# Kernel optimization log

Measured on AMD Instinct MI355X. Metric: run time of the kernel, lower is better.

Reference implementation:

```python
import jax, jax.numpy as jnp
import numpy as np

NCODONS = 100
ORDER = 2
ALPH = 4
N_STATES = 6 * NCODONS + 12            # calc_number_of_states()
N_TRANS = 3 * NCODONS + 5              # calc_number_of_transition_parameters()
N_EMIT_COLS = 6 ** (ORDER + 1)         # 216, per build()
N_OBS_SYMBOLS = (ALPH + 1) ** (ORDER + 1) + 1  # 126 order-transformed symbols


def _transition_structure(n):
    """Static sparse structure of the transition matrix (indices) and the
    delete-transition hop distances, exactly mirroring
    get_indices_and_values_from_transition_kernel_higher_order."""
    idx = [[0, 0], [0, 1], [1, 2], [2, 3]]
    idx += [[3 + i * 3, 4 + i * 3] for i in range(n)]
    idx += [[4 + i * 3, 5 + i * 3] for i in range(n)]
    idx += [[5 + i * 3, 6 + i * 3] for i in range(n)]
    off = 8 + 3 * n                      # first insert state
    idx += [[3 + i * 3, off + i * 3] for i in range(n + 1)]
    idx += [[3 + n * 3, 4 + n * 3]]
    idx += [[off + i * 3, off + 1 + i * 3] for i in range(n + 1)]
    idx += [[off + 1 + i * 3, off + 2 + i * 3] for i in range(n + 1)]
    idx += [[off + 2 + i * 3, 4 + i * 3] for i in range(n + 1)]
    idx += [[off + 2 + i * 3, off + i * 3] for i in range(n + 1)]
    i_del = [3 + i * 3 for i in range(n) for j in range(n - i)]
    j_del = [4 + j * 3 for i in range(1, n + 1) for j in range(i, n + 1)]
    idx += [[a, b] for a, b in zip(i_del, j_del)]
    idx += [[4 + n * 3, 5 + n * 3], [5 + n * 3, 6 + n * 3], [6 + n * 3, 7 + n * 3]]
    t1 = 8 + n * 3 + (n + 1) * 3         # terminal-1 state
    idx += [[7 + n * 3, 7 + n * 3], [7 + n * 3, t1], [t1, t1]]
    d = np.array([(b - a) // 3 for a, b in zip(i_del, j_del)], np.int32)
    return np.array(idx, np.int32), d

TRANS_IDX, DEL_HOPS = _transition_structure(NCODONS)


def _transition_values(w, n):
    """Values paired 1:1 with TRANS_IDX, same order as the original code."""
    wk = w[3 * n + 4]                    # shared delete parameter
    ones = lambda m: jnp.ones((m,), w.dtype)
    return jnp.concatenate([
        jnp.stack([1 - w[0], w[0]]),     # [0,0],[0,1]
        ones(2),                         # [1,2],[2,3]
        w[1:1 + n],                      # codon entries
        ones(2 * n),                     # codon chain x2
        w[1 + n:2 + 2 * n],              # inserts (n+1)
        w[2 + 2 * n:3 + 2 * n],          # last-codon -> stop
        ones(2 * (n + 1)),               # insert chains x2
        w[3 + 2 * n:4 + 3 * n],          # insert exit (n+1)
        1 - w[3 + 2 * n:4 + 3 * n],      # insert self-loop (n+1)
        1 - wk ** (jnp.asarray(DEL_HOPS) + 1),  # delete transitions
        ones(6),                         # stop chain + terminal loops
    ])


def make_A(transition_kernel):
    """Dense transition matrix after tf.sparse.softmax semantics:
    softmax over the structurally-nonzero entries of each row only."""
    vals = _transition_values(transition_kernel, NCODONS)
    logits = jnp.full((N_STATES, N_STATES), -jnp.inf, transition_kernel.dtype)
    logits = logits.at[TRANS_IDX[:, 0], TRANS_IDX[:, 1]].set(vals)
    return jax.nn.softmax(logits, axis=1)  # exp(-inf)=0 off-structure


def _forward_loglik(ids, transition_kernel, emission_kernel, init_kernel):
    A = make_A(transition_kernel)                                   # [S,S]
    E = jax.nn.softmax(emission_kernel.reshape(N_STATES, -1), axis=1)  # [S,216]
    Et = E.T                                                        # [216,S]
    pi = jax.nn.softmax(init_kernel)                                # [S]
    obs = ids.T                                                     # [T,B]

    a0 = pi[None, :] * Et[obs[0]]                                   # [B,S]
    s0 = a0.sum(-1, keepdims=True)
    carry0 = (a0 / s0, jnp.log(s0[..., 0]))

    def step(carry, ob):
        alpha, ll = carry
        a = (alpha @ A) * Et[ob]                                    # [B,S]
        s = a.sum(-1, keepdims=True)
        return (a / s, ll + jnp.log(s[..., 0])), None

    (alpha, ll), _ = jax.lax.scan(step, carry0, obs[1:])
    return ll                                                       # [B]


def setup_inputs() -> dict:
    key = jax.random.key(0)
    k1, k2, k3, k4 = jax.random.split(key, 4)
    ids = jax.random.randint(k1, (32, 2048), 0, N_OBS_SYMBOLS, dtype=jnp.int32)
    transition_kernel = 0.05 * jax.random.normal(k2, (N_TRANS,), jnp.float32)
    emission_kernel = 0.05 * jax.random.normal(k3, (N_STATES * N_EMIT_COLS,), jnp.float32)
    init_kernel = 0.05 * jax.random.normal(k4, (N_STATES,), jnp.float32)
    return {"ids": ids, "transition_kernel": transition_kernel,
            "emission_kernel": emission_kernel, "init_kernel": init_kernel}


def reference(ids, transition_kernel, emission_kernel, init_kernel):
    return _forward_loglik(ids, transition_kernel, emission_kernel, init_kernel)
```

## Files before the change

kernel.cpp:

```cpp
#include <hip/hip_runtime.h>
#include <math.h>

#define NS 612
#define NECOL 216
#define BATCH 32
#define TLEN 2048
#define ROWW 1024
#define CE 2.7182818284590452f

#define O_AV0 0
#define O_AV1 128
#define O_BV0 256
#define O_BV1 384
#define O_IZ3 512
#define O_SC  640
#define O_PIP 768
#define O_ET  2048

typedef float f32x4 __attribute__((ext_vector_type(4)));
typedef int   i32x2 __attribute__((ext_vector_type(2)));

__device__ __forceinline__ int eslot(int s) {
  if (s >= 4 && s <= 306)  { int i = (s - 4) / 3,  r = (s - 4) % 3;
    return (i >> 1) * 16 + (i & 1) * 6 + r; }
  if (s >= 308 && s <= 610){ int i = (s - 308) / 3, r = (s - 308) % 3;
    return (i >> 1) * 16 + (i & 1) * 6 + 3 + r; }
  if (s <= 3)   return (60 + s) * 16 + 12;
  if (s == 307) return 51 * 16 + 12;
  return 52 * 16 + 12;
}

#define DPPF(x, ctrl, rm) __int_as_float(__builtin_amdgcn_update_dpp(0, __float_as_int(x), (ctrl), (rm), 0xf, true))

__device__ __forceinline__ float scan_plain(float x) {
  x += DPPF(x, 0x111, 0xf);
  x += DPPF(x, 0x112, 0xf);
  x += DPPF(x, 0x114, 0xf);
  x += DPPF(x, 0x118, 0xf);
  x += DPPF(x, 0x142, 0xa);
  x += DPPF(x, 0x143, 0xc);
  return x;
}
__device__ __forceinline__ float wshr1(float x) { return DPPF(x, 0x138, 0xf); }
__device__ __forceinline__ float ror1(float x)  { return DPPF(x, 0x13C, 0xf); }
__device__ __forceinline__ float rdl(float x, int l) {
  return __int_as_float(__builtin_amdgcn_readlane(__float_as_int(x), l));
}

__global__ void k_prep(const float* __restrict__ w, float* __restrict__ ws) {
  __shared__ float Gs[101];
  int tid = threadIdx.x;
  float wk = w[304];
  if (tid >= 1 && tid <= 100) {
    float p = wk;
    for (int k = 0; k < tid; ++k) p *= wk;
    Gs[tid] = expf(1.f - p);
  }
  if (tid == 0) {
    Gs[0] = 0.f;
    ws[O_SC + 0] = wk;
    float Z0 = expf(1.f - w[0]) + expf(w[0]);
    ws[O_SC + 1] = expf(1.f - w[0]) / Z0;
    ws[O_SC + 2] = expf(w[0]) / Z0;
  }
  __syncthreads();
  if (tid <= 100) {
    float em = expf(w[tid < 100 ? 1 + tid : 202]);
    float ei = expf(w[101 + tid]);
    float z = em + ei;
    for (int d = 1; d <= 100 - tid; ++d) z += Gs[d];
    float ex = expf(w[203 + tid]);
    float es = expf(1.f - w[203 + tid]);
    float z310 = ex + es;
    ws[O_AV0 + tid] = em / z;
    ws[O_BV0 + tid] = ei / z;
    ws[O_AV1 + tid] = ex / z310;
    ws[O_BV1 + tid] = es / z310;
    ws[O_IZ3 + tid] = 1.f / z;
  }
}

__global__ void k_zr(float* __restrict__ ws) {
  float* row = ws + O_ET + (size_t)blockIdx.x * ROWW;
  for (int i = threadIdx.x; i < ROWW; i += 256) row[i] = 0.f;
}

__global__ void k_et(const float* __restrict__ ek, float* __restrict__ ws) {
  float* Etp = ws + O_ET;
  int s = blockIdx.x;
  int lane = threadIdx.x;
  int sl = eslot(s);
  float x[4]; float m = -1e30f;
  #pragma unroll
  for (int k = 0; k < 4; ++k) {
    int c = lane + 64 * k;
    x[k] = (c < NECOL) ? ek[s * NECOL + c] : -1e30f;
    m = fmaxf(m, x[k]);
  }
  #pragma unroll
  for (int o = 32; o; o >>= 1) m = fmaxf(m, __shfl_xor(m, o, 64));
  float e[4]; float sum = 0.f;
  #pragma unroll
  for (int k = 0; k < 4; ++k) {
    int c = lane + 64 * k;
    e[k] = (c < NECOL) ? expf(x[k] - m) : 0.f;
    sum += e[k];
  }
  #pragma unroll
  for (int o = 32; o; o >>= 1) sum += __shfl_xor(sum, o, 64);
  float inv = 1.f / sum;
  #pragma unroll
  for (int k = 0; k < 4; ++k) {
    int c = lane + 64 * k;
    if (c < NECOL) Etp[(size_t)c * ROWW + sl] = e[k] * inv;
  }
}

__global__ void k_pi(const float* __restrict__ ik, float* __restrict__ ws) {
  float* pip = ws + O_PIP;
  __shared__ float wm[10], wsm[10];
  int tid = threadIdx.x;
  for (int i = tid; i < ROWW; i += 640) pip[i] = 0.f;
  __syncthreads();
  int lane = tid & 63, wid = tid >> 6;
  float x = (tid < NS) ? ik[tid] : -1e30f;
  float m = x;
  #pragma unroll
  for (int o = 32; o; o >>= 1) m = fmaxf(m, __shfl_xor(m, o, 64));
  if (lane == 0) wm[wid] = m;
  __syncthreads();
  float mm = wm[0];
  #pragma unroll
  for (int k = 1; k < 10; ++k) mm = fmaxf(mm, wm[k]);
  float e = (tid < NS) ? expf(x - mm) : 0.f;
  float sacc = e;
  #pragma unroll
  for (int o = 32; o; o >>= 1) sacc += __shfl_xor(sacc, o, 64);
  if (lane == 0) wsm[wid] = sacc;
  __syncthreads();
  float ss = 0.f;
  #pragma unroll
  for (int k = 0; k < 10; ++k) ss += wsm[k];
  if (tid < NS) pip[eslot(tid)] = e / ss;
}

__global__ __launch_bounds__(64, 1) void k_main(const int* __restrict__ ids,
                                                const float* __restrict__ ws,
                                                float* __restrict__ out) {
  const int L = threadIdx.x, b = blockIdx.x;
  const int* idsb = ids + b * TLEN;
  const float* Etp = ws + O_ET;
  const float* pip = ws + O_PIP;
  const unsigned long long Et64 = (unsigned long long)Etp;
  const unsigned long long ids64 = (unsigned long long)idsb;
  const int voff = L << 6;

  int ie = 2 * L;     if (ie > 100) ie = 100;
  int io = 2 * L + 1; if (io > 100) io = 100;
  float AV0e = ws[O_AV0 + ie], AV1e = ws[O_AV1 + ie];
  float BV0e = ws[O_BV0 + ie], BV1e = ws[O_BV1 + ie];
  float AV0o = ws[O_AV0 + io], AV1o = ws[O_AV1 + io];
  float BV0o = ws[O_BV0 + io], BV1o = ws[O_BV1 + io];
  float izeCE = ((2 * L <= 99)     ? ws[O_IZ3 + 2 * L]     : 0.f) * CE;
  float izoCE = ((2 * L + 1 <= 99) ? ws[O_IZ3 + 2 * L + 1] : 0.f) * CE;
  float wk  = ws[O_SC + 0], A00 = ws[O_SC + 1], A01 = ws[O_SC + 2];

  float k0 = 0.f, k1 = 0.f, kx = 0.f;
  if (L == 61) k0 = A01;
  else if (L == 62 || L == 63) k0 = 1.f;
  else if (L == 52) k0 = 0.5f;
  if (L == 60) k1 = A00;
  else if (L == 51) { k1 = 0.5f; kx = 1.f; }
  else if (L == 52) k1 = 1.f;
  const bool isL0 = (L == 0);

  const float sk1 = 1.f - wk;
  const float r2 = wk * wk;
  const float q1 = r2, q2 = r2 * r2;

  int ob0 = __builtin_amdgcn_readfirstlane(idsb[0]);
  const float* R0 = Etp + (size_t)ob0 * ROWW;
  f32x4 p0 = *(const f32x4*)(pip + L * 16);
  f32x4 p1 = *(const f32x4*)(pip + L * 16 + 4);
  f32x4 p2 = *(const f32x4*)(pip + L * 16 + 8);
  float p3 = pip[L * 16 + 12];
  f32x4 e0 = *(const f32x4*)(R0 + L * 16);
  f32x4 e1 = *(const f32x4*)(R0 + L * 16 + 4);
  f32x4 e2 = *(const f32x4*)(R0 + L * 16 + 8);
  float e3 = R0[L * 16 + 12];

  float c4e = p0.x * e0.x, c5e = p0.y * e0.y, c6e = p0.z * e0.z, i8e = p0.w * e0.w;
  float i9e = p1.x * e1.x, i10e = p1.y * e1.y, c4o = p1.z * e1.z, c5o = p1.w * e1.w;
  float c6o = p2.x * e2.x, i8o = p2.y * e2.y, i9o = p2.z * e2.z, i10o = p2.w * e2.w;
  float spv = p3 * e3;

  float Sp, Tp, mdo;
  {
    float sprd0 = ror1(spv);
    float pme = isL0 ? sprd0 : ror1(c6o);
    float mde = pme * izeCE;
    mdo = c6e * izoCE;
    Sp = scan_plain(mde + mdo);
    float v1 = fmaf(wk, mde, mdo);
    float t1 = wshr1(v1), t2 = wshr1(t1);
    Tp = fmaf(q2, t2, fmaf(q1, t1, v1));
  }

  int e_acc = 0;

#define STEP_BODY(B0, B1, B2, B3) do { \
    float De = fmaf(-r2, wshr1(Tp), wshr1(Sp)); \
    float Do = fmaf(-wk, Tp, Sp); Do = fmaf(-sk1, mdo, Do); \
    float exc  = ror1(c6e); \
    float sprd = ror1(spv); \
    float pve = isL0 ? sprd : ror1(c6o); \
    float pvo = c6e; \
    float t4e = fmaf(AV0e, pve, fmaf(AV1e, i10e, De)) * (B0).x; \
    float t5e = c4e * (B0).y; \
    float t6e = c5e * (B0).z; \
    float t8e = fmaf(BV0e, pve, BV1e * i10e) * (B0).w; \
    float t9e = i8e * (B1).x; \
    float tXe = i9e * (B1).y; \
    float t4o = fmaf(AV0o, pvo, fmaf(AV1o, i10o, Do)) * (B1).z; \
    float t5o = c4o * (B1).w; \
    float t6o = c5o * (B2).x; \
    float t8o = fmaf(BV0o, pvo, BV1o * i10o) * (B2).y; \
    float t9o = i8o * (B2).z; \
    float tXo = i9o * (B2).w; \
    float nsp = fmaf(kx, exc, fmaf(k0, sprd, k1 * spv)) * (B3); \
    c4e = t4e; c5e = t5e; c6e = t6e; i8e = t8e; i9e = t9e; i10e = tXe; \
    c4o = t4o; c5o = t5o; c6o = t6o; i8o = t8o; i9o = t9o; i10o = tXo; \
    spv = nsp; \
    float sprdn = ror1(spv); \
    float pmn = isL0 ? sprdn : ror1(c6o); \
    float mde = pmn * izeCE; \
    mdo = c6e * izoCE; \
    Sp = scan_plain(mde + mdo); \
    float v1 = fmaf(wk, mde, mdo); \
    float t1 = wshr1(v1), t2 = wshr1(t1); \
    Tp = fmaf(q2, t2, fmaf(q1, t1, v1)); \
  } while (0)

#define FUSE2(R1a, R1b, R1c, R1d, R2a, R2b, R2c, R2d) do { \
     \
    float De = fmaf(-r2, wshr1(Tp), wshr1(Sp)); \
    float Do = fmaf(-wk, Tp, Sp); Do = fmaf(-sk1, mdo, Do); \
    float exc  = ror1(c6e); \
    float sprd = ror1(spv); \
    float pve = isL0 ? sprd : ror1(c6o); \
    float pvo = c6e; \
    float a4e = fmaf(AV0e, pve, fmaf(AV1e, i10e, De)) * (R1a).x; \
    float a5e = c4e * (R1a).y; \
    float a6e = c5e * (R1a).z; \
    float a8e = fmaf(BV0e, pve, BV1e * i10e) * (R1a).w; \
    float a9e = i8e * (R1b).x; \
    float aXe = i9e * (R1b).y; \
    float a4o = fmaf(AV0o, pvo, fmaf(AV1o, i10o, Do)) * (R1b).z; \
    float a5o = c4o * (R1b).w; \
    float a6o = c5o * (R1c).x; \
    float a8o = fmaf(BV0o, pvo, BV1o * i10o) * (R1c).y; \
    float a9o = i8o * (R1c).z; \
    float aXo = i9o * (R1c).w; \
    float asp = fmaf(kx, exc, fmaf(k0, sprd, k1 * spv)) * (R1d); \
     \
    float b5e = a4e * (R2a).y; \
    float b6e = a5e * (R2a).z; \
    float b9e = a8e * (R2b).x; \
    float bXe = a9e * (R2b).y; \
    float b5o = a4o * (R2b).w; \
    float b6o = a5o * (R2c).x; \
    float b9o = a8o * (R2c).z; \
    float bXo = a9o * (R2c).w; \
    float excb  = ror1(a6e); \
    float bsprd = ror1(asp); \
    float bsp = fmaf(kx, excb, fmaf(k0, bsprd, k1 * asp)) * (R2d); \
    float pma = isL0 ? bsprd : ror1(a6o); \
    float mdea = pma * izeCE; \
    float mdoa = a6e * izoCE; \
    float csprd = ror1(bsp); \
    float pmb = isL0 ? csprd : ror1(b6o); \
    float mdeb = pmb * izeCE; \
    float mdob = b6e * izoCE; \
    float Sa = mdea + mdoa, Ta0 = fmaf(wk, mdea, mdoa); \
    float Sb = mdeb + mdob, Tb0 = fmaf(wk, mdeb, mdob); \
     \
    Sa += DPPF(Sa, 0x111, 0xf); Sb += DPPF(Sb, 0x111, 0xf); \
    float ta1 = wshr1(Ta0); float tb1 = wshr1(Tb0); \
    Sa += DPPF(Sa, 0x112, 0xf); Sb += DPPF(Sb, 0x112, 0xf); \
    float ta2 = wshr1(ta1); float tb2 = wshr1(tb1); \
    Sa += DPPF(Sa, 0x114, 0xf); Sb += DPPF(Sb, 0x114, 0xf); \
    float Ta = fmaf(q2, ta2, fmaf(q1, ta1, Ta0)); \
    float Tb = fmaf(q2, tb2, fmaf(q1, tb1, Tb0)); \
    Sa += DPPF(Sa, 0x118, 0xf); Sb += DPPF(Sb, 0x118, 0xf); \
    Sa += DPPF(Sa, 0x142, 0xa); Sb += DPPF(Sb, 0x142, 0xa); \
    Sa += DPPF(Sa, 0x143, 0xc); Sb += DPPF(Sb, 0x143, 0xc); \
     \
    float Deb = fmaf(-r2, wshr1(Ta), wshr1(Sa)); \
    float Dob = fmaf(-wk, Ta, Sa); Dob = fmaf(-sk1, mdoa, Dob); \
    float b4e = fmaf(AV0e, pma, fmaf(AV1e, aXe, Deb)) * (R2a).x; \
    float b8e = fmaf(BV0e, pma, BV1e * aXe) * (R2a).w; \
    float b4o = fmaf(AV0o, a6e, fmaf(AV1o, aXo, Dob)) * (R2b).z; \
    float b8o = fmaf(BV0o, a6e, BV1o * aXo) * (R2c).y; \
     \
    c4e = b4e; c5e = b5e; c6e = b6e; i8e = b8e; i9e = b9e; i10e = bXe; \
    c4o = b4o; c5o = b5o; c6o = b6o; i8o = b8o; i9o = b9o; i10o = bXo; \
    spv = bsp; \
    Sp = Sb; Tp = Tb; mdo = mdob; \
  } while (0)

#define RESCALE() do { \
    float prr = ((c4e + c5e) + (c6e + i8e)) + ((i9e + i10e) + (c4o + c5o)) \
              + ((c6o + i8o) + (i9o + i10o)) + spv; \
    float ssum = rdl(scan_plain(prr), 63); \
    int exq = ((__float_as_int(ssum) >> 23) & 255) - 127; \
    e_acc += exq; \
    float scq = __int_as_float((127 - exq) << 23); \
    c4e *= scq; c5e *= scq; c6e *= scq; i8e *= scq; i9e *= scq; i10e *= scq; \
    c4o *= scq; c5o *= scq; c6o *= scq; i8o *= scq; i9o *= scq; i10o *= scq; \
    spv *= scq; \
    mdo *= scq; Sp *= scq; Tp *= scq; \
  } while (0)

#define GLD4(dst, base, off) \
  asm volatile("global_load_dwordx4 %0, %1, %2 offset:" #off \
               : "=v"(dst) : "v"(voff), "s"(base))
#define GLD1(dst, base, off) \
  asm volatile("global_load_dword %0, %1, %2 offset:" #off \
               : "=v"(dst) : "v"(voff), "s"(base))
#define GLD2(dst, base, vo, off) \
  asm volatile("global_load_dwordx2 %0, %1, %2 offset:" #off \
               : "=v"(dst) : "v"(vo), "s"(base))

#define LOADROW(P, obsv) do { \
    unsigned int _oc = (unsigned int)__builtin_amdgcn_readfirstlane(obsv); \
    unsigned long long _ba = Et64 + ((unsigned long long)_oc << 12); \
    GLD4(P##0, _ba, 0); \
    GLD4(P##1, _ba, 16); \
    GLD4(P##2, _ba, 32); \
    GLD1(P##3, _ba, 48); \
  } while (0)

#define LOADOBS(O, tstart) do { \
    int _ts = (tstart); if (_ts > TLEN - 6) _ts = TLEN - 6; \
    int _vo = _ts * 4; \
    GLD2(O##0, ids64, _vo, 0); \
    GLD2(O##1, ids64, _vo, 8); \
    GLD2(O##2, ids64, _vo, 16); \
  } while (0)

  for (int t = 1; t <= 7; ++t) {
    int obp = idsb[t];
    const float* Rx = Etp + (size_t)__builtin_amdgcn_readfirstlane(obp) * ROWW;
    f32x4 P0 = *(const f32x4*)(Rx + L * 16);
    f32x4 P1 = *(const f32x4*)(Rx + L * 16 + 4);
    f32x4 P2 = *(const f32x4*)(Rx + L * 16 + 8);
    float P3 = Rx[L * 16 + 12];
    STEP_BODY(P0, P1, P2, P3);
  }
  RESCALE();

  f32x4 Ar00, Ar01, Ar02; float Ar03;
  f32x4 Ar10, Ar11, Ar12; float Ar13;
  f32x4 Ar20, Ar21, Ar22; float Ar23;
  f32x4 Ar30, Ar31, Ar32; float Ar33;
  f32x4 Ar40, Ar41, Ar42; float Ar43;
  f32x4 Ar50, Ar51, Ar52; float Ar53;
  f32x4 Br00, Br01, Br02; float Br03;
  f32x4 Br10, Br11, Br12; float Br13;
  f32x4 Br20, Br21, Br22; float Br23;
  f32x4 Br30, Br31, Br32; float Br33;
  f32x4 Br40, Br41, Br42; float Br43;
  f32x4 Br50, Br51, Br52; float Br53;
  i32x2 OA0, OA1, OA2, OB0, OB1, OB2;

  LOADOBS(OA, 8);
  asm volatile("s_waitcnt vmcnt(0)" ::: "memory");
  __builtin_amdgcn_sched_barrier(0);
  LOADROW(Ar0, OA0.x);
  LOADROW(Ar1, OA0.y);
  LOADROW(Ar2, OA1.x);
  LOADROW(Ar3, OA1.y);
  LOADROW(Ar4, OA2.x);
  LOADROW(Ar5, OA2.y);
  LOADOBS(OB, 14);

#define ITER(C, OC, N, ON, gexp) do { \
    asm volatile("s_waitcnt vmcnt(0)" ::: "memory"); \
    __builtin_amdgcn_sched_barrier(0); \
    LOADROW(N##r0, (OC##0).x); \
    LOADROW(N##r1, (OC##0).y); \
    LOADROW(N##r2, (OC##1).x); \
    LOADROW(N##r3, (OC##1).y); \
    LOADROW(N##r4, (OC##2).x); \
    LOADROW(N##r5, (OC##2).y); \
    LOADOBS(ON, 8 + 6 * ((gexp) + 2)); \
    __builtin_amdgcn_sched_barrier(0); \
    FUSE2(C##r00, C##r01, C##r02, C##r03, C##r10, C##r11, C##r12, C##r13); \
    FUSE2(C##r20, C##r21, C##r22, C##r23, C##r30, C##r31, C##r32, C##r33); \
    FUSE2(C##r40, C##r41, C##r42, C##r43, C##r50, C##r51, C##r52, C##r53); \
  } while (0)

  for (int g = 0; g < 340; g += 2) {
    ITER(A, OB, B, OA, g);
    ITER(B, OA, A, OB, g + 1);
    RESCALE();
  }

  float prr = ((c4e + c5e) + (c6e + i8e)) + ((i9e + i10e) + (c4o + c5o))
            + ((c6o + i8o) + (i9o + i10o)) + spv;
  float ssum_f = rdl(scan_plain(prr), 63);
  double ll = (double)e_acc * 0.6931471805599453 + (double)logf(ssum_f);
  if (L == 0) out[b] = (float)ll;

#undef STEP_BODY
#undef FUSE2
#undef RESCALE
#undef GLD4
#undef GLD1
#undef GLD2
#undef LOADROW
#undef LOADOBS
#undef ITER
}

extern "C" void kernel_launch(void* const* d_in, const int* in_sizes, int n_in,
                              void* d_out, int out_size, void* d_ws, size_t ws_size,
                              hipStream_t stream) {
  const int*   ids = (const int*)d_in[0];
  const float* w   = (const float*)d_in[1];
  const float* ek  = (const float*)d_in[2];
  const float* ik  = (const float*)d_in[3];
  float* ws  = (float*)d_ws;
  float* out = (float*)d_out;

  k_prep<<<1, 128, 0, stream>>>(w, ws);
  k_zr  <<<NECOL, 256, 0, stream>>>(ws);
  k_pi  <<<1, 640, 0, stream>>>(ik, ws);
  k_et  <<<NS, 64, 0, stream>>>(ek, ws);
  k_main<<<BATCH, 64, 0, stream>>>(ids, ws, out);
}
```

Before: 299.0 us.

## Fuse three HMM time steps per block to batch the cross-lane scans

Replaces the two-step fused forward update with a three-step fusion. The three delete-path prefix scans (DPP adds and lane shifts) now run interleaved in one batch instead of two, which gives the serial dependency chain more instruction-level parallelism. The cost is higher register pressure from more live temporaries, and the step ordering is more intricate to get right.

```diff
diff --git a/kernel.cpp b/kernel.cpp
--- a/kernel.cpp
+++ b/kernel.cpp
@@ -241,27 +241,26 @@
     Tp = fmaf(q2, t2, fmaf(q1, t1, v1)); \
   } while (0)
 
-#define FUSE2(R1a, R1b, R1c, R1d, R2a, R2b, R2c, R2d) do { \
-     \
-    float De = fmaf(-r2, wshr1(Tp), wshr1(Sp)); \
-    float Do = fmaf(-wk, Tp, Sp); Do = fmaf(-sk1, mdo, Do); \
-    float exc  = ror1(c6e); \
-    float sprd = ror1(spv); \
-    float pve = isL0 ? sprd : ror1(c6o); \
-    float pvo = c6e; \
-    float a4e = fmaf(AV0e, pve, fmaf(AV1e, i10e, De)) * (R1a).x; \
+#define FUSE3(R1a,R1b,R1c,R1d, R2a,R2b,R2c,R2d, R3a,R3b,R3c,R3d) do { \
+     \
+    float De1 = fmaf(-r2, wshr1(Tp), wshr1(Sp)); \
+    float Do1 = fmaf(-wk, Tp, Sp); Do1 = fmaf(-sk1, mdo, Do1); \
+    float exc1  = ror1(c6e); \
+    float sprd1 = ror1(spv); \
+    float pve1 = isL0 ? sprd1 : ror1(c6o); \
+    float a4e = fmaf(AV0e, pve1, fmaf(AV1e, i10e, De1)) * (R1a).x; \
     float a5e = c4e * (R1a).y; \
     float a6e = c5e * (R1a).z; \
-    float a8e = fmaf(BV0e, pve, BV1e * i10e) * (R1a).w; \
+    float a8e = fmaf(BV0e, pve1, BV1e * i10e) * (R1a).w; \
     float a9e = i8e * (R1b).x; \
     float aXe = i9e * (R1b).y; \
-    float a4o = fmaf(AV0o, pvo, fmaf(AV1o, i10o, Do)) * (R1b).z; \
+    float a4o = fmaf(AV0o, c6e, fmaf(AV1o, i10o, Do1)) * (R1b).z; \
     float a5o = c4o * (R1b).w; \
     float a6o = c5o * (R1c).x; \
-    float a8o = fmaf(BV0o, pvo, BV1o * i10o) * (R1c).y; \
+    float a8o = fmaf(BV0o, c6e, BV1o * i10o) * (R1c).y; \
     float a9o = i8o * (R1c).z; \
     float aXo = i9o * (R1c).w; \
-    float asp = fmaf(kx, exc, fmaf(k0, sprd, k1 * spv)) * (R1d); \
+    float asp = fmaf(kx, exc1, fmaf(k0, sprd1, k1 * spv)) * (R1d); \
      \
     float b5e = a4e * (R2a).y; \
     float b6e = a5e * (R2a).z; \
@@ -271,41 +270,64 @@
     float b6o = a5o * (R2c).x; \
     float b9o = a8o * (R2c).z; \
     float bXo = a9o * (R2c).w; \
-    float excb  = ror1(a6e); \
-    float bsprd = ror1(asp); \
-    float bsp = fmaf(kx, excb, fmaf(k0, bsprd, k1 * asp)) * (R2d); \
-    float pma = isL0 ? bsprd : ror1(a6o); \
-    float mdea = pma * izeCE; \
-    float mdoa = a6e * izoCE; \
-    float csprd = ror1(bsp); \
-    float pmb = isL0 ? csprd : ror1(b6o); \
-    float mdeb = pmb * izeCE; \
-    float mdob = b6e * izoCE; \
-    float Sa = mdea + mdoa, Ta0 = fmaf(wk, mdea, mdoa); \
-    float Sb = mdeb + mdob, Tb0 = fmaf(wk, mdeb, mdob); \
-     \
-    Sa += DPPF(Sa, 0x111, 0xf); Sb += DPPF(Sb, 0x111, 0xf); \
-    float ta1 = wshr1(Ta0); float tb1 = wshr1(Tb0); \
-    Sa += DPPF(Sa, 0x112, 0xf); Sb += DPPF(Sb, 0x112, 0xf); \
-    float ta2 = wshr1(ta1); float tb2 = wshr1(tb1); \
-    Sa += DPPF(Sa, 0x114, 0xf); Sb += DPPF(Sb, 0x114, 0xf); \
-    float Ta = fmaf(q2, ta2, fmaf(q1, ta1, Ta0)); \
-    float Tb = fmaf(q2, tb2, fmaf(q1, tb1, Tb0)); \
-    Sa += DPPF(Sa, 0x118, 0xf); Sb += DPPF(Sb, 0x118, 0xf); \
-    Sa += DPPF(Sa, 0x142, 0xa); Sb += DPPF(Sb, 0x142, 0xa); \
-    Sa += DPPF(Sa, 0x143, 0xc); Sb += DPPF(Sb, 0x143, 0xc); \
-     \
-    float Deb = fmaf(-r2, wshr1(Ta), wshr1(Sa)); \
-    float Dob = fmaf(-wk, Ta, Sa); Dob = fmaf(-sk1, mdoa, Dob); \
-    float b4e = fmaf(AV0e, pma, fmaf(AV1e, aXe, Deb)) * (R2a).x; \
-    float b8e = fmaf(BV0e, pma, BV1e * aXe) * (R2a).w; \
-    float b4o = fmaf(AV0o, a6e, fmaf(AV1o, aXo, Dob)) * (R2b).z; \
+    float exc2  = ror1(a6e); \
+    float sprd2 = ror1(asp); \
+    float bsp = fmaf(kx, exc2, fmaf(k0, sprd2, k1 * asp)) * (R2d); \
+    float pve2 = isL0 ? sprd2 : ror1(a6o); \
+    float b8e = fmaf(BV0e, pve2, BV1e * aXe) * (R2a).w; \
     float b8o = fmaf(BV0o, a6e, BV1o * aXo) * (R2c).y; \
-     \
-    c4e = b4e; c5e = b5e; c6e = b6e; i8e = b8e; i9e = b9e; i10e = bXe; \
-    c4o = b4o; c5o = b5o; c6o = b6o; i8o = b8o; i9o = b9o; i10o = bXo; \
-    spv = bsp; \
-    Sp = Sb; Tp = Tb; mdo = mdob; \
+    float md1e = pve2 * izeCE; \
+    float md1o = a6e * izoCE; \
+     \
+    float c6e3 = b5e * (R3a).z; \
+    float c6o3 = b5o * (R3c).x; \
+    float c9e3 = b8e * (R3b).x; \
+    float cXe3 = b9e * (R3b).y; \
+    float c9o3 = b8o * (R3c).z; \
+    float cXo3 = b9o * (R3c).w; \
+    float exc3  = ror1(b6e); \
+    float sprd3 = ror1(bsp); \
+    float csp = fmaf(kx, exc3, fmaf(k0, sprd3, k1 * bsp)) * (R3d); \
+    float pve3 = isL0 ? sprd3 : ror1(b6o); \
+    float md2e = pve3 * izeCE; \
+    float md2o = b6e * izoCE; \
+    float c8e3 = fmaf(BV0e, pve3, BV1e * bXe) * (R3a).w; \
+    float c8o3 = fmaf(BV0o, b6e, BV1o * bXo) * (R3c).y; \
+    float sprd4 = ror1(csp); \
+    float pm3 = isL0 ? sprd4 : ror1(c6o3); \
+    float md3e = pm3 * izeCE; \
+    float md3o = c6e3 * izoCE; \
+     \
+    float S1 = md1e + md1o, T1v = fmaf(wk, md1e, md1o); \
+    float S2 = md2e + md2o, T2v = fmaf(wk, md2e, md2o); \
+    float S3 = md3e + md3o, T3v = fmaf(wk, md3e, md3o); \
+    S1 += DPPF(S1, 0x111, 0xf); S2 += DPPF(S2, 0x111, 0xf); S3 += DPPF(S3, 0x111, 0xf); \
+    float t1a = wshr1(T1v), t2a = wshr1(T2v), t3a = wshr1(T3v); \
+    S1 += DPPF(S1, 0x112, 0xf); S2 += DPPF(S2, 0x112, 0xf); S3 += DPPF(S3, 0x112, 0xf); \
+    float t1b = wshr1(t1a), t2b = wshr1(t2a), t3b = wshr1(t3a); \
+    S1 += DPPF(S1, 0x114, 0xf); S2 += DPPF(S2, 0x114, 0xf); S3 += DPPF(S3, 0x114, 0xf); \
+    float T1 = fmaf(q2, t1b, fmaf(q1, t1a, T1v)); \
+    float T2 = fmaf(q2, t2b, fmaf(q1, t2a, T2v)); \
+    float T3 = fmaf(q2, t3b, fmaf(q1, t3a, T3v)); \
+    S1 += DPPF(S1, 0x118, 0xf); S2 += DPPF(S2, 0x118, 0xf); S3 += DPPF(S3, 0x118, 0xf); \
+    S1 += DPPF(S1, 0x142, 0xa); S2 += DPPF(S2, 0x142, 0xa); S3 += DPPF(S3, 0x142, 0xa); \
+    S1 += DPPF(S1, 0x143, 0xc); S2 += DPPF(S2, 0x143, 0xc); S3 += DPPF(S3, 0x143, 0xc); \
+     \
+    float De2 = fmaf(-r2, wshr1(T1), wshr1(S1)); \
+    float Do2 = fmaf(-wk, T1, S1); Do2 = fmaf(-sk1, md1o, Do2); \
+    float b4e = fmaf(AV0e, pve2, fmaf(AV1e, aXe, De2)) * (R2a).x; \
+    float b4o = fmaf(AV0o, a6e, fmaf(AV1o, aXo, Do2)) * (R2b).z; \
+    float c5e3 = b4e * (R3a).y; \
+    float c5o3 = b4o * (R3b).w; \
+    float De3 = fmaf(-r2, wshr1(T2), wshr1(S2)); \
+    float Do3 = fmaf(-wk, T2, S2); Do3 = fmaf(-sk1, md2o, Do3); \
+    float c4e3 = fmaf(AV0e, pve3, fmaf(AV1e, bXe, De3)) * (R3a).x; \
+    float c4o3 = fmaf(AV0o, b6e, fmaf(AV1o, bXo, Do3)) * (R3b).z; \
+     \
+    c4e = c4e3; c5e = c5e3; c6e = c6e3; i8e = c8e3; i9e = c9e3; i10e = cXe3; \
+    c4o = c4o3; c5o = c5o3; c6o = c6o3; i8o = c8o3; i9o = c9o3; i10o = cXo3; \
+    spv = csp; \
+    Sp = S3; Tp = T3; mdo = md3o; \
   } while (0)
 
 #define RESCALE() do { \
@@ -395,9 +417,12 @@
     LOADROW(N##r5, (OC##2).y); \
     LOADOBS(ON, 8 + 6 * ((gexp) + 2)); \
     __builtin_amdgcn_sched_barrier(0); \
-    FUSE2(C##r00, C##r01, C##r02, C##r03, C##r10, C##r11, C##r12, C##r13); \
-    FUSE2(C##r20, C##r21, C##r22, C##r23, C##r30, C##r31, C##r32, C##r33); \
-    FUSE2(C##r40, C##r41, C##r42, C##r43, C##r50, C##r51, C##r52, C##r53); \
+    FUSE3(C##r00, C##r01, C##r02, C##r03, \
+          C##r10, C##r11, C##r12, C##r13, \
+          C##r20, C##r21, C##r22, C##r23); \
+    FUSE3(C##r30, C##r31, C##r32, C##r33, \
+          C##r40, C##r41, C##r42, C##r43, \
+          C##r50, C##r51, C##r52, C##r53); \
   } while (0)
 
   for (int g = 0; g < 340; g += 2) {
@@ -413,7 +438,7 @@
   if (L == 0) out[b] = (float)ll;
 
 #undef STEP_BODY
-#undef FUSE2
+#undef FUSE3
 #undef RESCALE
 #undef GLD4
 #undef GLD1
```

New measurement: 294.0 us. Within noise of the previous version (-1.7%).

## Interleave even/odd codon slots and use packed f32x2 FMA math

Applied to the files above, without the earlier changes.

Reorders the per-lane emission/state slot layout so each even/odd codon pair sits in adjacent floats. The recurrence then runs on f32x2 vectors that can map to packed FP32 instructions (v_pk_fma/v_pk_mul) on CDNA3/4, roughly halving VALU op count on the serial critical path. The packing may add shuffle/mov overhead when building pairs (mk2) that cancels part of the gain.

```diff
diff --git a/kernel.cpp b/kernel.cpp
--- a/kernel.cpp
+++ b/kernel.cpp
@@ -18,19 +18,25 @@
 #define O_ET  2048
 
 typedef float f32x4 __attribute__((ext_vector_type(4)));
+typedef float f32x2 __attribute__((ext_vector_type(2)));
 typedef int   i32x2 __attribute__((ext_vector_type(2)));
 
 __device__ __forceinline__ int eslot(int s) {
   if (s >= 4 && s <= 306)  { int i = (s - 4) / 3,  r = (s - 4) % 3;
-    return (i >> 1) * 16 + (i & 1) * 6 + r; }
+    return (i >> 1) * 16 + 2 * r + (i & 1); }
   if (s >= 308 && s <= 610){ int i = (s - 308) / 3, r = (s - 308) % 3;
-    return (i >> 1) * 16 + (i & 1) * 6 + 3 + r; }
+    return (i >> 1) * 16 + 6 + 2 * r + (i & 1); }
   if (s <= 3)   return (60 + s) * 16 + 12;
   if (s == 307) return 51 * 16 + 12;
   return 52 * 16 + 12;
 }
 
 #define DPPF(x, ctrl, rm) __int_as_float(__builtin_amdgcn_update_dpp(0, __float_as_int(x), (ctrl), (rm), 0xf, true))
+#define LO2(v) __builtin_shufflevector((v), (v), 0, 1)
+#define HI2(v) __builtin_shufflevector((v), (v), 2, 3)
+#define PKF(a, b, c) __builtin_elementwise_fma((a), (b), (c))
+
+__device__ __forceinline__ f32x2 mk2(float a, float b) { f32x2 r; r.x = a; r.y = b; return r; }
 
 __device__ __forceinline__ float scan_plain(float x) {
   x += DPPF(x, 0x111, 0xf);
@@ -157,12 +163,12 @@
 
   int ie = 2 * L;     if (ie > 100) ie = 100;
   int io = 2 * L + 1; if (io > 100) io = 100;
-  float AV0e = ws[O_AV0 + ie], AV1e = ws[O_AV1 + ie];
-  float BV0e = ws[O_BV0 + ie], BV1e = ws[O_BV1 + ie];
-  float AV0o = ws[O_AV0 + io], AV1o = ws[O_AV1 + io];
-  float BV0o = ws[O_BV0 + io], BV1o = ws[O_BV1 + io];
-  float izeCE = ((2 * L <= 99)     ? ws[O_IZ3 + 2 * L]     : 0.f) * CE;
-  float izoCE = ((2 * L + 1 <= 99) ? ws[O_IZ3 + 2 * L + 1] : 0.f) * CE;
+  f32x2 AV0p = mk2(ws[O_AV0 + ie], ws[O_AV0 + io]);
+  f32x2 AV1p = mk2(ws[O_AV1 + ie], ws[O_AV1 + io]);
+  f32x2 BV0p = mk2(ws[O_BV0 + ie], ws[O_BV0 + io]);
+  f32x2 BV1p = mk2(ws[O_BV1 + ie], ws[O_BV1 + io]);
+  f32x2 IZp  = mk2(((2 * L <= 99)     ? ws[O_IZ3 + 2 * L]     : 0.f) * CE,
+                   ((2 * L + 1 <= 99) ? ws[O_IZ3 + 2 * L + 1] : 0.f) * CE);
   float wk  = ws[O_SC + 0], A00 = ws[O_SC + 1], A01 = ws[O_SC + 2];
 
   float k0 = 0.f, k1 = 0.f, kx = 0.f;
@@ -189,101 +195,88 @@
   f32x4 e2 = *(const f32x4*)(R0 + L * 16 + 8);
   float e3 = R0[L * 16 + 12];
 
-  float c4e = p0.x * e0.x, c5e = p0.y * e0.y, c6e = p0.z * e0.z, i8e = p0.w * e0.w;
-  float i9e = p1.x * e1.x, i10e = p1.y * e1.y, c4o = p1.z * e1.z, c5o = p1.w * e1.w;
-  float c6o = p2.x * e2.x, i8o = p2.y * e2.y, i9o = p2.z * e2.z, i10o = p2.w * e2.w;
+  f32x2 C4 = LO2(p0) * LO2(e0);
+  f32x2 C5 = HI2(p0) * HI2(e0);
+  f32x2 C6 = LO2(p1) * LO2(e1);
+  f32x2 I8 = HI2(p1) * HI2(e1);
+  f32x2 I9 = LO2(p2) * LO2(e2);
+  f32x2 I10 = HI2(p2) * HI2(e2);
   float spv = p3 * e3;
 
   float Sp, Tp, mdo;
   {
     float sprd0 = ror1(spv);
-    float pme = isL0 ? sprd0 : ror1(c6o);
-    float mde = pme * izeCE;
-    mdo = c6e * izoCE;
-    Sp = scan_plain(mde + mdo);
-    float v1 = fmaf(wk, mde, mdo);
+    float pme = isL0 ? sprd0 : ror1(C6.y);
+    f32x2 MD = mk2(pme, C6.x) * IZp;
+    mdo = MD.y;
+    Sp = scan_plain(MD.x + MD.y);
+    float v1 = fmaf(wk, MD.x, MD.y);
     float t1 = wshr1(v1), t2 = wshr1(t1);
     Tp = fmaf(q2, t2, fmaf(q1, t1, v1));
   }
 
   int e_acc = 0;
 
-#define STEP_BODY(B0, B1, B2, B3) do { \
+#define STEP_BODY(Ra, Rb, Rc, Rd) do { \
     float De = fmaf(-r2, wshr1(Tp), wshr1(Sp)); \
     float Do = fmaf(-wk, Tp, Sp); Do = fmaf(-sk1, mdo, Do); \
-    float exc  = ror1(c6e); \
+    f32x2 Dp = mk2(De, Do); \
+    float exc  = ror1(C6.x); \
     float sprd = ror1(spv); \
-    float pve = isL0 ? sprd : ror1(c6o); \
-    float pvo = c6e; \
-    float t4e = fmaf(AV0e, pve, fmaf(AV1e, i10e, De)) * (B0).x; \
-    float t5e = c4e * (B0).y; \
-    float t6e = c5e * (B0).z; \
-    float t8e = fmaf(BV0e, pve, BV1e * i10e) * (B0).w; \
-    float t9e = i8e * (B1).x; \
-    float tXe = i9e * (B1).y; \
-    float t4o = fmaf(AV0o, pvo, fmaf(AV1o, i10o, Do)) * (B1).z; \
-    float t5o = c4o * (B1).w; \
-    float t6o = c5o * (B2).x; \
-    float t8o = fmaf(BV0o, pvo, BV1o * i10o) * (B2).y; \
-    float t9o = i8o * (B2).z; \
-    float tXo = i9o * (B2).w; \
-    float nsp = fmaf(kx, exc, fmaf(k0, sprd, k1 * spv)) * (B3); \
-    c4e = t4e; c5e = t5e; c6e = t6e; i8e = t8e; i9e = t9e; i10e = tXe; \
-    c4o = t4o; c5o = t5o; c6o = t6o; i8o = t8o; i9o = t9o; i10o = tXo; \
-    spv = nsp; \
+    float pve = isL0 ? sprd : ror1(C6.y); \
+    f32x2 PV = mk2(pve, C6.x); \
+    f32x2 T4 = PKF(AV0p, PV, PKF(AV1p, I10, Dp)) * LO2(Ra); \
+    f32x2 T5 = C4 * HI2(Ra); \
+    f32x2 T6 = C5 * LO2(Rb); \
+    f32x2 T8 = PKF(BV0p, PV, BV1p * I10) * HI2(Rb); \
+    f32x2 T9 = I8 * LO2(Rc); \
+    f32x2 TX = I9 * HI2(Rc); \
+    float nsp = fmaf(kx, exc, fmaf(k0, sprd, k1 * spv)) * (Rd); \
+    C4 = T4; C5 = T5; C6 = T6; I8 = T8; I9 = T9; I10 = TX; spv = nsp; \
     float sprdn = ror1(spv); \
-    float pmn = isL0 ? sprdn : ror1(c6o); \
-    float mde = pmn * izeCE; \
-    mdo = c6e * izoCE; \
-    Sp = scan_plain(mde + mdo); \
-    float v1 = fmaf(wk, mde, mdo); \
+    float pmn = isL0 ? sprdn : ror1(C6.y); \
+    f32x2 MD = mk2(pmn, C6.x) * IZp; \
+    mdo = MD.y; \
+    Sp = scan_plain(MD.x + MD.y); \
+    float v1 = fmaf(wk, MD.x, MD.y); \
     float t1 = wshr1(v1), t2 = wshr1(t1); \
     Tp = fmaf(q2, t2, fmaf(q1, t1, v1)); \
   } while (0)
 
-#define FUSE2(R1a, R1b, R1c, R1d, R2a, R2b, R2c, R2d) do { \
+#define FUSE2P(R1a, R1b, R1c, R1d, R2a, R2b, R2c, R2d) do { \
      \
     float De = fmaf(-r2, wshr1(Tp), wshr1(Sp)); \
     float Do = fmaf(-wk, Tp, Sp); Do = fmaf(-sk1, mdo, Do); \
-    float exc  = ror1(c6e); \
-    float sprd = ror1(spv); \
-    float pve = isL0 ? sprd : ror1(c6o); \
-    float pvo = c6e; \
-    float a4e = fmaf(AV0e, pve, fmaf(AV1e, i10e, De)) * (R1a).x; \
-    float a5e = c4e * (R1a).y; \
-    float a6e = c5e * (R1a).z; \
-    float a8e = fmaf(BV0e, pve, BV1e * i10e) * (R1a).w; \
-    float a9e = i8e * (R1b).x; \
-    float aXe = i9e * (R1b).y; \
-    float a4o = fmaf(AV0o, pvo, fmaf(AV1o, i10o, Do)) * (R1b).z; \
-    float a5o = c4o * (R1b).w; \
-    float a6o = c5o * (R1c).x; \
-    float a8o = fmaf(BV0o, pvo, BV1o * i10o) * (R1c).y; \
-    float a9o = i8o * (R1c).z; \
-    float aXo = i9o * (R1c).w; \
-    float asp = fmaf(kx, exc, fmaf(k0, sprd, k1 * spv)) * (R1d); \
+    f32x2 Dp = mk2(De, Do); \
+    float exc1  = ror1(C6.x); \
+    float sprd1 = ror1(spv); \
+    float pve1 = isL0 ? sprd1 : ror1(C6.y); \
+    f32x2 PV1 = mk2(pve1, C6.x); \
+    f32x2 A4 = PKF(AV0p, PV1, PKF(AV1p, I10, Dp)) * LO2(R1a); \
+    f32x2 A5 = C4 * HI2(R1a); \
+    f32x2 A6 = C5 * LO2(R1b); \
+    f32x2 A8 = PKF(BV0p, PV1, BV1p * I10) * HI2(R1b); \
+    f32x2 A9 = I8 * LO2(R1c); \
+    f32x2 AX = I9 * HI2(R1c); \
+    float asp = fmaf(kx, exc1, fmaf(k0, sprd1, k1 * spv)) * (R1d); \
      \
-    float b5e = a4e * (R2a).y; \
-    float b6e = a5e * (R2a).z; \
-    float b9e = a8e * (R2b).x; \
-    float bXe = a9e * (R2b).y; \
-    float b5o = a4o * (R2b).w; \
-    float b6o = a5o * (R2c).x; \
-    float b9o = a8o * (R2c).z; \
-    float bXo = a9o * (R2c).w; \
-    float excb  = ror1(a6e); \
-    float bsprd = ror1(asp); \
-    float bsp = fmaf(kx, excb, fmaf(k0, bsprd, k1 * asp)) * (R2d); \
-    float pma = isL0 ? bsprd : ror1(a6o); \
-    float mdea = pma * izeCE; \
-    float mdoa = a6e * izoCE; \
-    float csprd = ror1(bsp); \
-    float pmb = isL0 ? csprd : ror1(b6o); \
-    float mdeb = pmb * izeCE; \
-    float mdob = b6e * izoCE; \
-    float Sa = mdea + mdoa, Ta0 = fmaf(wk, mdea, mdoa); \
-    float Sb = mdeb + mdob, Tb0 = fmaf(wk, mdeb, mdob); \
+    f32x2 B5 = A4 * HI2(R2a); \
+    f32x2 B6 = A5 * LO2(R2b); \
+    f32x2 B9 = A8 * LO2(R2c); \
+    f32x2 BX = A9 * HI2(R2c); \
+    float exc2  = ror1(A6.x); \
+    float sprd2 = ror1(asp); \
+    float bsp = fmaf(kx, exc2, fmaf(k0, sprd2, k1 * asp)) * (R2d); \
+    float pve2 = isL0 ? sprd2 : ror1(A6.y); \
+    f32x2 PV2 = mk2(pve2, A6.x); \
+    f32x2 B8 = PKF(BV0p, PV2, BV1p * AX) * HI2(R2b); \
+    f32x2 MD1 = PV2 * IZp; \
+    float sprd3 = ror1(bsp); \
+    float pm3 = isL0 ? sprd3 : ror1(B6.y); \
+    f32x2 MD2 = mk2(pm3, B6.x) * IZp; \
      \
+    float Sa = MD1.x + MD1.y, Ta0 = fmaf(wk, MD1.x, MD1.y); \
+    float Sb = MD2.x + MD2.y, Tb0 = fmaf(wk, MD2.x, MD2.y); \
     Sa += DPPF(Sa, 0x111, 0xf); Sb += DPPF(Sb, 0x111, 0xf); \
     float ta1 = wshr1(Ta0); float tb1 = wshr1(Tb0); \
     Sa += DPPF(Sa, 0x112, 0xf); Sb += DPPF(Sb, 0x112, 0xf); \
@@ -295,28 +288,24 @@
     Sa += DPPF(Sa, 0x142, 0xa); Sb += DPPF(Sb, 0x142, 0xa); \
     Sa += DPPF(Sa, 0x143, 0xc); Sb += DPPF(Sb, 0x143, 0xc); \
      \
-    float Deb = fmaf(-r2, wshr1(Ta), wshr1(Sa)); \
-    float Dob = fmaf(-wk, Ta, Sa); Dob = fmaf(-sk1, mdoa, Dob); \
-    float b4e = fmaf(AV0e, pma, fmaf(AV1e, aXe, Deb)) * (R2a).x; \
-    float b8e = fmaf(BV0e, pma, BV1e * aXe) * (R2a).w; \
-    float b4o = fmaf(AV0o, a6e, fmaf(AV1o, aXo, Dob)) * (R2b).z; \
-    float b8o = fmaf(BV0o, a6e, BV1o * aXo) * (R2c).y; \
+    float De2 = fmaf(-r2, wshr1(Ta), wshr1(Sa)); \
+    float Do2 = fmaf(-wk, Ta, Sa); Do2 = fmaf(-sk1, MD1.y, Do2); \
+    f32x2 D2p = mk2(De2, Do2); \
+    f32x2 B4 = PKF(AV0p, PV2, PKF(AV1p, AX, D2p)) * LO2(R2a); \
      \
-    c4e = b4e; c5e = b5e; c6e = b6e; i8e = b8e; i9e = b9e; i10e = bXe; \
-    c4o = b4o; c5o = b5o; c6o = b6o; i8o = b8o; i9o = b9o; i10o = bXo; \
-    spv = bsp; \
-    Sp = Sb; Tp = Tb; mdo = mdob; \
+    C4 = B4; C5 = B5; C6 = B6; I8 = B8; I9 = B9; I10 = BX; spv = bsp; \
+    Sp = Sb; Tp = Tb; mdo = MD2.y; \
   } while (0)
 
 #define RESCALE() do { \
-    float prr = ((c4e + c5e) + (c6e + i8e)) + ((i9e + i10e) + (c4o + c5o)) \
-              + ((c6o + i8o) + (i9o + i10o)) + spv; \
+    f32x2 Psum = ((C4 + C5) + (C6 + I8)) + (I9 + I10); \
+    float prr = (Psum.x + Psum.y) + spv; \
     float ssum = rdl(scan_plain(prr), 63); \
     int exq = ((__float_as_int(ssum) >> 23) & 255) - 127; \
     e_acc += exq; \
     float scq = __int_as_float((127 - exq) << 23); \
-    c4e *= scq; c5e *= scq; c6e *= scq; i8e *= scq; i9e *= scq; i10e *= scq; \
-    c4o *= scq; c5o *= scq; c6o *= scq; i8o *= scq; i9o *= scq; i10o *= scq; \
+    f32x2 SC = mk2(scq, scq); \
+    C4 *= SC; C5 *= SC; C6 *= SC; I8 *= SC; I9 *= SC; I10 *= SC; \
     spv *= scq; \
     mdo *= scq; Sp *= scq; Tp *= scq; \
   } while (0)
@@ -395,9 +384,9 @@
     LOADROW(N##r5, (OC##2).y); \
     LOADOBS(ON, 8 + 6 * ((gexp) + 2)); \
     __builtin_amdgcn_sched_barrier(0); \
-    FUSE2(C##r00, C##r01, C##r02, C##r03, C##r10, C##r11, C##r12, C##r13); \
-    FUSE2(C##r20, C##r21, C##r22, C##r23, C##r30, C##r31, C##r32, C##r33); \
-    FUSE2(C##r40, C##r41, C##r42, C##r43, C##r50, C##r51, C##r52, C##r53); \
+    FUSE2P(C##r00, C##r01, C##r02, C##r03, C##r10, C##r11, C##r12, C##r13); \
+    FUSE2P(C##r20, C##r21, C##r22, C##r23, C##r30, C##r31, C##r32, C##r33); \
+    FUSE2P(C##r40, C##r41, C##r42, C##r43, C##r50, C##r51, C##r52, C##r53); \
   } while (0)
 
   for (int g = 0; g < 340; g += 2) {
@@ -406,14 +395,14 @@
     RESCALE();
   }
 
-  float prr = ((c4e + c5e) + (c6e + i8e)) + ((i9e + i10e) + (c4o + c5o))
-            + ((c6o + i8o) + (i9o + i10o)) + spv;
+  f32x2 Psum = ((C4 + C5) + (C6 + I8)) + (I9 + I10);
+  float prr = (Psum.x + Psum.y) + spv;
   float ssum_f = rdl(scan_plain(prr), 63);
   double ll = (double)e_acc * 0.6931471805599453 + (double)logf(ssum_f);
   if (L == 0) out[b] = (float)ll;
 
 #undef STEP_BODY
-#undef FUSE2
+#undef FUSE2P
 #undef RESCALE
 #undef GLD4
 #undef GLD1
```

Measured after the change: 266.6 us. -10.8%, faster.
